# Performance work log

Measured on AMD Instinct MI355X. Metric: run time of the kernel, lower is better.

## Reference

```python
import jax, jax.numpy as jnp
import numpy as np

N_NODES = 100000
N_EDGES = 1600000
IN_DIM = 64
OUT_DIM = 64
BN_EPS = 1e-5


def batchnorm(h, gamma, beta):
    # BatchNorm1d in training mode: per-feature batch stats, biased variance
    mean = jnp.mean(h, axis=0)
    var = jnp.mean((h - mean) ** 2, axis=0)
    return gamma * (h - mean) * jax.lax.rsqrt(var + BN_EPS) + beta


def setup_inputs() -> dict:
    key = jax.random.key(0)
    ks = jax.random.split(key, 4)
    x = jax.random.normal(ks[0], (N_NODES, IN_DIM), dtype=jnp.float32)
    edge_index = jax.random.randint(ks[1], (2, N_EDGES), 0, N_NODES, dtype=jnp.int32)
    epsilon = jnp.asarray(0.1, dtype=jnp.float32)
    # Linear weights stored [in, out] (transpose of torch layout)
    W1 = jax.random.normal(ks[2], (IN_DIM, 2 * OUT_DIM), dtype=jnp.float32) * (1.0 / np.sqrt(IN_DIM))
    b1 = jnp.zeros((2 * OUT_DIM,), dtype=jnp.float32)
    g1 = jnp.ones((2 * OUT_DIM,), dtype=jnp.float32)
    be1 = jnp.zeros((2 * OUT_DIM,), dtype=jnp.float32)
    W2 = jax.random.normal(ks[3], (2 * OUT_DIM, OUT_DIM), dtype=jnp.float32) * (1.0 / np.sqrt(2 * OUT_DIM))
    b2 = jnp.zeros((OUT_DIM,), dtype=jnp.float32)
    g2 = jnp.ones((OUT_DIM,), dtype=jnp.float32)
    be2 = jnp.zeros((OUT_DIM,), dtype=jnp.float32)
    return {"x": x, "edge_index": edge_index, "epsilon": epsilon,
            "W1": W1, "b1": b1, "g1": g1, "be1": be1,
            "W2": W2, "b2": b2, "g2": g2, "be2": be2}


def reference(x, edge_index, epsilon, W1, b1, g1, be1, W2, b2, g2, be2):
    src, dst = edge_index[0], edge_index[1]
    # gather messages from src, scatter-add into dst  [N, D]
    neighbor_sum = jnp.zeros_like(x).at[dst].add(x[src])
    combined = (1.0 + epsilon) * x + neighbor_sum
    h = combined @ W1 + b1            # [N, 2*out_dim]
    h = jax.nn.relu(batchnorm(h, g1, be1))
    h = h @ W2 + b2                   # [N, out_dim]
    return batchnorm(h, g2, be2)
```

## Files before the change

kernel.cpp:

```cpp
#include <hip/hip_runtime.h>

#define N_NODES 100000
#define N_EDGES 1600000
#define IN_DIM 64
#define H_DIM 128
#define OUT_DIM 64
#define BN_EPS 1e-5f
#define CAP 64
#define BIN_SHIFT 9
#define BIN_NODES 512
#define NB 256
#define NBIN_BLOCKS ((N_NODES + BIN_NODES - 1) / BIN_NODES)

#define OFF_XB    0
#define OFF_COMB  3200000
#define OFF_H1    6400000
#define OFF_H2    12800000
#define OFF_STATS 19200000
#define S1SUM 0
#define S1SQ  128
#define S2SUM 256
#define S2SQ  320
#define STATS_FLOATS 768

#define DEV_ATOMIC_ADD(p, v) __hip_atomic_fetch_add((p), (v), __ATOMIC_RELAXED, __HIP_MEMORY_SCOPE_AGENT)

typedef __attribute__((ext_vector_type(8))) short short8;
typedef __attribute__((ext_vector_type(4))) float f32x4;

__device__ __forceinline__ unsigned short f2bf(float f) {
  union { float f; unsigned u; } v; v.f = f;
  unsigned r = v.u + 0x7FFFu + ((v.u >> 16) & 1u);
  return (unsigned short)(r >> 16);
}
__device__ __forceinline__ float bflo(unsigned v) { union { unsigned u; float f; } t; t.u = v << 16; return t.f; }
__device__ __forceinline__ float bfhi(unsigned v) { union { unsigned u; float f; } t; t.u = v & 0xFFFF0000u; return t.f; }

__global__ __launch_bounds__(256) void k_cvt(const float* __restrict__ x,
                                             unsigned short* __restrict__ xb) {
  int i = blockIdx.x * 256 + threadIdx.x;
  if (i < N_NODES * IN_DIM / 4) {
    float4 v = ((const float4*)x)[i];
    ushort4 o;
    o.x = f2bf(v.x); o.y = f2bf(v.y); o.z = f2bf(v.z); o.w = f2bf(v.w);
    *(ushort4*)(xb + i * 4) = o;
  }
}

__global__ __launch_bounds__(256) void k_bhist(const int* __restrict__ ei,
                                               int* __restrict__ bhist) {
  __shared__ int h[NB];
  const int tid = threadIdx.x;
  h[tid] = 0;
  __syncthreads();
  #pragma unroll
  for (int j = 0; j < 8; ++j) {
    int e = blockIdx.x * 2048 + j * 256 + tid;
    if (e < N_EDGES) atomicAdd(&h[ei[N_EDGES + e] >> BIN_SHIFT], 1);
  }
  __syncthreads();
  if (h[tid]) DEV_ATOMIC_ADD(&bhist[tid], h[tid]);
}

__global__ __launch_bounds__(256) void k_scan256(const int* __restrict__ bhist,
                                                 int* __restrict__ boff,
                                                 int* __restrict__ bcur) {
  __shared__ int s[NB];
  const int tid = threadIdx.x;
  int v = bhist[tid];
  s[tid] = v;
  __syncthreads();
  for (int d = 1; d < NB; d <<= 1) {
    int t = (tid >= d) ? s[tid - d] : 0;
    __syncthreads();
    s[tid] += t;
    __syncthreads();
  }
  int incl = s[tid];
  boff[tid] = incl - v;
  if (tid == NB - 1) boff[NB] = incl;
  bcur[tid] = incl - v;
}

__global__ __launch_bounds__(256) void k_bsplit(const int* __restrict__ ei,
                                                int* __restrict__ bcur,
                                                int2* __restrict__ binned) {
  __shared__ int lcnt[NB];
  __shared__ int lbase[NB];
  const int tid = threadIdx.x;
  lcnt[tid] = 0;
  __syncthreads();
  int src[8], dst[8], rk[8];
  #pragma unroll
  for (int j = 0; j < 8; ++j) {
    int e = blockIdx.x * 2048 + j * 256 + tid;
    if (e < N_EDGES) {
      src[j] = ei[e];
      dst[j] = ei[N_EDGES + e];
      rk[j] = atomicAdd(&lcnt[dst[j] >> BIN_SHIFT], 1);
    } else {
      src[j] = -1;
    }
  }
  __syncthreads();
  int c = lcnt[tid];
  if (c > 0) lbase[tid] = DEV_ATOMIC_ADD(&bcur[tid], c);
  __syncthreads();
  #pragma unroll
  for (int j = 0; j < 8; ++j) {
    if (src[j] >= 0) {
      int b = dst[j] >> BIN_SHIFT;
      binned[lbase[b] + rk[j]] = make_int2(src[j], dst[j]);
    }
  }
}

__global__ __launch_bounds__(512) void k_bfill(const int* __restrict__ boff,
                                               const int2* __restrict__ binned,
                                               int* __restrict__ cnt,
                                               int* __restrict__ srcl) {
  __shared__ int lcnt[BIN_NODES];
  const int tid = threadIdx.x;
  for (int i = tid; i < BIN_NODES; i += 512) lcnt[i] = 0;
  __syncthreads();
  const int b = blockIdx.x;
  const int s = boff[b], e = boff[b + 1];
  const int base = b * BIN_NODES;
  for (int i = s + tid; i < e; i += 512) {
    int2 ed = binned[i];
    int pos = atomicAdd(&lcnt[ed.y - base], 1);
    if (pos < CAP) srcl[ed.y * CAP + pos] = ed.x;
  }
  __syncthreads();
  for (int i = tid; i < BIN_NODES; i += 512) {
    int node = base + i;
    if (node < N_NODES) cnt[node] = lcnt[i];
  }
}

__global__ __launch_bounds__(256) void k_gather(const unsigned short* __restrict__ xb,
                                                const float* __restrict__ eps,
                                                const int* __restrict__ cnt,
                                                const int* __restrict__ srcl,
                                                unsigned short* __restrict__ comb) {
  int gid = blockIdx.x * 256 + threadIdx.x;
  int node = gid >> 3;
  int c = gid & 7;
  if (node >= N_NODES) return;
  float e = 1.0f + eps[0];
  uint4 u = *(const uint4*)(xb + node * 64 + c * 8);
  float a0 = bflo(u.x) * e, a1 = bfhi(u.x) * e;
  float a2 = bflo(u.y) * e, a3 = bfhi(u.y) * e;
  float a4 = bflo(u.z) * e, a5 = bfhi(u.z) * e;
  float a6 = bflo(u.w) * e, a7 = bfhi(u.w) * e;
  int deg = cnt[node];
  if (deg > CAP) deg = CAP;
  const int* sl = srcl + node * CAP;
  for (int j = 0; j < deg; ++j) {
    int s = sl[j];
    uint4 v = *(const uint4*)(xb + s * 64 + c * 8);
    a0 += bflo(v.x); a1 += bfhi(v.x);
    a2 += bflo(v.y); a3 += bfhi(v.y);
    a4 += bflo(v.z); a5 += bfhi(v.z);
    a6 += bflo(v.w); a7 += bfhi(v.w);
  }
  uint4 o;
  o.x = (unsigned)f2bf(a0) | ((unsigned)f2bf(a1) << 16);
  o.y = (unsigned)f2bf(a2) | ((unsigned)f2bf(a3) << 16);
  o.z = (unsigned)f2bf(a4) | ((unsigned)f2bf(a5) << 16);
  o.w = (unsigned)f2bf(a6) | ((unsigned)f2bf(a7) << 16);
  *(uint4*)(comb + node * 64 + c * 8) = o;
}

#define APAD 72
__global__ __launch_bounds__(256) void k_gemm1(const unsigned short* __restrict__ comb,
                                               const float* __restrict__ W1,
                                               const float* __restrict__ b1,
                                               unsigned short* __restrict__ h1,
                                               float* __restrict__ stats) {
  __shared__ unsigned short As[128 * APAD];
  __shared__ unsigned short Ws[128 * APAD];
  __shared__ float red[4][128];
  const int tid = threadIdx.x;
  const int wv = tid >> 6, lane = tid & 63;
  const int quad = lane >> 4, ln = lane & 15;
  const int rowBase = blockIdx.x * 128;

  #pragma unroll
  for (int it = 0; it < 4; ++it) {
    int idx = it * 256 + tid;
    int row = idx >> 3, ch = idx & 7;
    int gRow = rowBase + row;
    uint4 v = (gRow < N_NODES) ? *(const uint4*)(comb + gRow * 64 + ch * 8)
                               : make_uint4(0, 0, 0, 0);
    *(uint4*)&As[row * APAD + ch * 8] = v;
  }
  #pragma unroll
  for (int it = 0; it < 8; ++it) {
    int idx = it * 256 + tid;
    int k = idx >> 5, n4 = idx & 31;
    float4 wv1 = *(const float4*)(W1 + k * 128 + n4 * 4);
    Ws[(n4 * 4 + 0) * APAD + k] = f2bf(wv1.x);
    Ws[(n4 * 4 + 1) * APAD + k] = f2bf(wv1.y);
    Ws[(n4 * 4 + 2) * APAD + k] = f2bf(wv1.z);
    Ws[(n4 * 4 + 3) * APAD + k] = f2bf(wv1.w);
  }
  __syncthreads();

  f32x4 acc[2][8];
  #pragma unroll
  for (int mt = 0; mt < 2; ++mt) {
    #pragma unroll
    for (int nt = 0; nt < 8; ++nt) acc[mt][nt] = (f32x4)0.0f;
  }

  const int rw = wv * 32;
  #pragma unroll
  for (int kb = 0; kb < 2; ++kb) {
    short8 a0 = *(short8*)&As[(rw + ln) * APAD + kb * 32 + quad * 8];
    short8 a1 = *(short8*)&As[(rw + 16 + ln) * APAD + kb * 32 + quad * 8];
    #pragma unroll
    for (int nt = 0; nt < 8; ++nt) {
      short8 b = *(short8*)&Ws[(nt * 16 + ln) * APAD + kb * 32 + quad * 8];
      acc[0][nt] = __builtin_amdgcn_mfma_f32_16x16x32_bf16(a0, b, acc[0][nt], 0, 0, 0);
      acc[1][nt] = __builtin_amdgcn_mfma_f32_16x16x32_bf16(a1, b, acc[1][nt], 0, 0, 0);
    }
  }

  float bias[8], s[8], q[8];
  #pragma unroll
  for (int nt = 0; nt < 8; ++nt) { bias[nt] = b1[nt * 16 + ln]; s[nt] = 0.f; q[nt] = 0.f; }
  #pragma unroll
  for (int mt = 0; mt < 2; ++mt) {
    #pragma unroll
    for (int i = 0; i < 4; ++i) {
      int gRow = rowBase + rw + mt * 16 + quad * 4 + i;
      if (gRow < N_NODES) {
        #pragma unroll
        for (int nt = 0; nt < 8; ++nt) {
          float v = acc[mt][nt][i] + bias[nt];
          h1[gRow * 128 + nt * 16 + ln] = f2bf(v);
          s[nt] += v; q[nt] += v * v;
        }
      }
    }
  }
  #pragma unroll
  for (int nt = 0; nt < 8; ++nt) {
    s[nt] += __shfl_xor(s[nt], 16); s[nt] += __shfl_xor(s[nt], 32);
    q[nt] += __shfl_xor(q[nt], 16); q[nt] += __shfl_xor(q[nt], 32);
  }
  if (lane < 16) {
    #pragma unroll
    for (int nt = 0; nt < 8; ++nt) red[wv][nt * 16 + ln] = s[nt];
  }
  __syncthreads();
  if (tid < 128) DEV_ATOMIC_ADD(&stats[S1SUM + tid],
                                red[0][tid] + red[1][tid] + red[2][tid] + red[3][tid]);
  __syncthreads();
  if (lane < 16) {
    #pragma unroll
    for (int nt = 0; nt < 8; ++nt) red[wv][nt * 16 + ln] = q[nt];
  }
  __syncthreads();
  if (tid < 128) DEV_ATOMIC_ADD(&stats[S1SQ + tid],
                                red[0][tid] + red[1][tid] + red[2][tid] + red[3][tid]);
}

#define WPAD 136
__global__ __launch_bounds__(256) void k_gemm2(const unsigned short* __restrict__ h1,
                                               const float* __restrict__ W2,
                                               const float* __restrict__ b2,
                                               const float* __restrict__ g1,
                                               const float* __restrict__ be1,
                                               float* __restrict__ h2,
                                               float* __restrict__ stats) {
  __shared__ unsigned short As[128 * APAD];
  __shared__ unsigned short Ws[64 * WPAD];
  __shared__ float red[4][64];
  __shared__ float scL[128], shL[128];
  const int tid = threadIdx.x;
  const int wv = tid >> 6, lane = tid & 63;
  const int quad = lane >> 4, ln = lane & 15;
  const int rowBase = blockIdx.x * 128;

  if (tid < 128) {
    float mean = stats[S1SUM + tid] * (1.0f / N_NODES);
    float var = stats[S1SQ + tid] * (1.0f / N_NODES) - mean * mean;
    var = fmaxf(var, 0.0f);
    float sc = g1[tid] * rsqrtf(var + BN_EPS);
    scL[tid] = sc;
    shL[tid] = be1[tid] - mean * sc;
  }
  #pragma unroll
  for (int it = 0; it < 8; ++it) {
    int idx = it * 256 + tid;
    int k = idx >> 4, n4 = idx & 15;
    float4 wv2 = *(const float4*)(W2 + k * 64 + n4 * 4);
    Ws[(n4 * 4 + 0) * WPAD + k] = f2bf(wv2.x);
    Ws[(n4 * 4 + 1) * WPAD + k] = f2bf(wv2.y);
    Ws[(n4 * 4 + 2) * WPAD + k] = f2bf(wv2.z);
    Ws[(n4 * 4 + 3) * WPAD + k] = f2bf(wv2.w);
  }

  f32x4 acc[2][4];
  #pragma unroll
  for (int mt = 0; mt < 2; ++mt) {
    #pragma unroll
    for (int nt = 0; nt < 4; ++nt) acc[mt][nt] = (f32x4)0.0f;
  }
  const int rw = wv * 32;

  for (int kc = 0; kc < 2; ++kc) {
    __syncthreads();
    #pragma unroll
    for (int it = 0; it < 4; ++it) {
      int idx = it * 256 + tid;
      int row = idx >> 3, ch = idx & 7;
      int gRow = rowBase + row;
      uint4 u = (gRow < N_NODES) ? *(const uint4*)(h1 + gRow * 128 + kc * 64 + ch * 8)
                                 : make_uint4(0, 0, 0, 0);
      int kb = kc * 64 + ch * 8;
      float f0 = fmaxf(bflo(u.x) * scL[kb + 0] + shL[kb + 0], 0.f);
      float f1 = fmaxf(bfhi(u.x) * scL[kb + 1] + shL[kb + 1], 0.f);
      float f2 = fmaxf(bflo(u.y) * scL[kb + 2] + shL[kb + 2], 0.f);
      float f3 = fmaxf(bfhi(u.y) * scL[kb + 3] + shL[kb + 3], 0.f);
      float f4 = fmaxf(bflo(u.z) * scL[kb + 4] + shL[kb + 4], 0.f);
      float f5 = fmaxf(bfhi(u.z) * scL[kb + 5] + shL[kb + 5], 0.f);
      float f6 = fmaxf(bflo(u.w) * scL[kb + 6] + shL[kb + 6], 0.f);
      float f7 = fmaxf(bfhi(u.w) * scL[kb + 7] + shL[kb + 7], 0.f);
      uint4 o;
      o.x = (unsigned)f2bf(f0) | ((unsigned)f2bf(f1) << 16);
      o.y = (unsigned)f2bf(f2) | ((unsigned)f2bf(f3) << 16);
      o.z = (unsigned)f2bf(f4) | ((unsigned)f2bf(f5) << 16);
      o.w = (unsigned)f2bf(f6) | ((unsigned)f2bf(f7) << 16);
      *(uint4*)&As[row * APAD + ch * 8] = o;
    }
    __syncthreads();
    #pragma unroll
    for (int kb = 0; kb < 2; ++kb) {
      short8 a0 = *(short8*)&As[(rw + ln) * APAD + kb * 32 + quad * 8];
      short8 a1 = *(short8*)&As[(rw + 16 + ln) * APAD + kb * 32 + quad * 8];
      #pragma unroll
      for (int nt = 0; nt < 4; ++nt) {
        short8 b = *(short8*)&Ws[(nt * 16 + ln) * WPAD + kc * 64 + kb * 32 + quad * 8];
        acc[0][nt] = __builtin_amdgcn_mfma_f32_16x16x32_bf16(a0, b, acc[0][nt], 0, 0, 0);
        acc[1][nt] = __builtin_amdgcn_mfma_f32_16x16x32_bf16(a1, b, acc[1][nt], 0, 0, 0);
      }
    }
  }

  float bias[4], s[4], q[4];
  #pragma unroll
  for (int nt = 0; nt < 4; ++nt) { bias[nt] = b2[nt * 16 + ln]; s[nt] = 0.f; q[nt] = 0.f; }
  #pragma unroll
  for (int mt = 0; mt < 2; ++mt) {
    #pragma unroll
    for (int i = 0; i < 4; ++i) {
      int gRow = rowBase + rw + mt * 16 + quad * 4 + i;
      if (gRow < N_NODES) {
        #pragma unroll
        for (int nt = 0; nt < 4; ++nt) {
          float v = acc[mt][nt][i] + bias[nt];
          h2[gRow * 64 + nt * 16 + ln] = v;
          s[nt] += v; q[nt] += v * v;
        }
      }
    }
  }
  #pragma unroll
  for (int nt = 0; nt < 4; ++nt) {
    s[nt] += __shfl_xor(s[nt], 16); s[nt] += __shfl_xor(s[nt], 32);
    q[nt] += __shfl_xor(q[nt], 16); q[nt] += __shfl_xor(q[nt], 32);
  }
  if (lane < 16) {
    #pragma unroll
    for (int nt = 0; nt < 4; ++nt) red[wv][nt * 16 + ln] = s[nt];
  }
  __syncthreads();
  if (tid < 64) DEV_ATOMIC_ADD(&stats[S2SUM + tid],
                               red[0][tid] + red[1][tid] + red[2][tid] + red[3][tid]);
  __syncthreads();
  if (lane < 16) {
    #pragma unroll
    for (int nt = 0; nt < 4; ++nt) red[wv][nt * 16 + ln] = q[nt];
  }
  __syncthreads();
  if (tid < 64) DEV_ATOMIC_ADD(&stats[S2SQ + tid],
                               red[0][tid] + red[1][tid] + red[2][tid] + red[3][tid]);
}

__global__ __launch_bounds__(256) void k_out(const float* __restrict__ h2,
                                             const float* __restrict__ stats,
                                             const float* __restrict__ g2,
                                             const float* __restrict__ be2,
                                             float* __restrict__ out) {
  __shared__ float scL[64], shL[64];
  const int tid = threadIdx.x;
  if (tid < 64) {
    float mean = stats[S2SUM + tid] * (1.0f / N_NODES);
    float var = stats[S2SQ + tid] * (1.0f / N_NODES) - mean * mean;
    var = fmaxf(var, 0.0f);
    float sc = g2[tid] * rsqrtf(var + BN_EPS);
    scL[tid] = sc;
    shL[tid] = be2[tid] - mean * sc;
  }
  __syncthreads();
  int i = blockIdx.x * 256 + tid;
  if (i < N_NODES * OUT_DIM / 4) {
    int c = i & 15;
    float4 v = ((const float4*)h2)[i];
    float4 sc = ((const float4*)scL)[c];
    float4 sh = ((const float4*)shL)[c];
    v.x = v.x * sc.x + sh.x;
    v.y = v.y * sc.y + sh.y;
    v.z = v.z * sc.z + sh.z;
    v.w = v.w * sc.w + sh.w;
    ((float4*)out)[i] = v;
  }
}

extern "C" void kernel_launch(void* const* d_in, const int* in_sizes, int n_in,
                              void* d_out, int out_size, void* d_ws, size_t ws_size,
                              hipStream_t stream) {
  const float* x   = (const float*)d_in[0];
  const int*   ei  = (const int*)d_in[1];
  const float* eps = (const float*)d_in[2];
  const float* W1  = (const float*)d_in[3];
  const float* b1  = (const float*)d_in[4];
  const float* g1  = (const float*)d_in[5];
  const float* be1 = (const float*)d_in[6];
  const float* W2  = (const float*)d_in[7];
  const float* b2  = (const float*)d_in[8];
  const float* g2  = (const float*)d_in[9];
  const float* be2 = (const float*)d_in[10];

  float* ws = (float*)d_ws;
  unsigned short* xb   = (unsigned short*)(ws + OFF_XB);
  unsigned short* comb = (unsigned short*)(ws + OFF_COMB);
  int2*           binned = (int2*)(ws + OFF_COMB);
  unsigned short* h1   = (unsigned short*)(ws + OFF_H1);
  int*            srcl = (int*)(ws + OFF_H1);
  float*          h2   = ws + OFF_H2;
  int*            cnt  = (int*)(ws + OFF_H2);
  int*            bhist = cnt + N_NODES;
  int*            boff  = bhist + NB;
  int*            bcur  = boff + NB + 7;
  float*          stats = ws + OFF_STATS;
  float*          out   = (float*)d_out;

  hipMemsetAsync(stats, 0, STATS_FLOATS * sizeof(float), stream);
  hipMemsetAsync(bhist, 0, NB * sizeof(int), stream);

  const int edgeGrid = (N_EDGES + 2047) / 2048;
  const int gemmGrid = (N_NODES + 127) / 128;
  k_cvt<<<(N_NODES * IN_DIM / 4 + 255) / 256, 256, 0, stream>>>(x, xb);
  k_bhist<<<edgeGrid, 256, 0, stream>>>(ei, bhist);
  k_scan256<<<1, NB, 0, stream>>>(bhist, boff, bcur);
  k_bsplit<<<edgeGrid, 256, 0, stream>>>(ei, bcur, binned);
  k_bfill<<<NBIN_BLOCKS, 512, 0, stream>>>(boff, binned, cnt, srcl);
  k_gather<<<(N_NODES * 8 + 255) / 256, 256, 0, stream>>>(xb, eps, cnt, srcl, comb);
  k_gemm1<<<gemmGrid, 256, 0, stream>>>(comb, W1, b1, h1, stats);
  k_gemm2<<<gemmGrid, 256, 0, stream>>>(h1, W2, b2, g1, be1, h2, stats);
  k_out<<<(N_NODES * OUT_DIM / 4 + 255) / 256, 256, 0, stream>>>(h2, stats, g2, be2, out);
}
```

Before: 282.0 us.

## Stage binned edges in LDS, widen gather lanes, store h2 in bf16

k_bsplit now writes its edges into shared memory sorted by bin via a local prefix scan, then copies them out, so global writes of binned edges are grouped by bin and more contiguous. k_gather uses 4 threads per node with 32-byte loads and handles two neighbours per loop iteration, which cuts thread count and raises the number of loads in flight per thread. The second GEMM writes h2 as bf16 instead of fp32, and k_out reads bf16, halving the traffic of that intermediate. The costs are lower precision in the pre-BN2 output, extra shared-memory scan work in bsplit, and more registers in gather.

```diff
diff --git a/kernel.cpp b/kernel.cpp
--- a/kernel.cpp
+++ b/kernel.cpp
@@ -36,6 +36,19 @@
 __device__ __forceinline__ float bflo(unsigned v) { union { unsigned u; float f; } t; t.u = v << 16; return t.f; }
 __device__ __forceinline__ float bfhi(unsigned v) { union { unsigned u; float f; } t; t.u = v & 0xFFFF0000u; return t.f; }
 
+__device__ __forceinline__ void acc8(float* a, uint4 v) {
+  a[0] += bflo(v.x); a[1] += bfhi(v.x); a[2] += bflo(v.y); a[3] += bfhi(v.y);
+  a[4] += bflo(v.z); a[5] += bfhi(v.z); a[6] += bflo(v.w); a[7] += bfhi(v.w);
+}
+__device__ __forceinline__ uint4 pack8(const float* a) {
+  uint4 o;
+  o.x = (unsigned)f2bf(a[0]) | ((unsigned)f2bf(a[1]) << 16);
+  o.y = (unsigned)f2bf(a[2]) | ((unsigned)f2bf(a[3]) << 16);
+  o.z = (unsigned)f2bf(a[4]) | ((unsigned)f2bf(a[5]) << 16);
+  o.w = (unsigned)f2bf(a[6]) | ((unsigned)f2bf(a[7]) << 16);
+  return o;
+}
+
 __global__ __launch_bounds__(256) void k_cvt(const float* __restrict__ x,
                                              unsigned short* __restrict__ xb) {
   int i = blockIdx.x * 256 + threadIdx.x;
@@ -86,7 +99,10 @@
                                                 int* __restrict__ bcur,
                                                 int2* __restrict__ binned) {
   __shared__ int lcnt[NB];
+  __shared__ int lofs[NB];
   __shared__ int lbase[NB];
+  __shared__ int sc[NB];
+  __shared__ int2 staged[2048];
   const int tid = threadIdx.x;
   lcnt[tid] = 0;
   __syncthreads();
@@ -103,15 +119,31 @@
     }
   }
   __syncthreads();
-  int c = lcnt[tid];
-  if (c > 0) lbase[tid] = DEV_ATOMIC_ADD(&bcur[tid], c);
+  int v = lcnt[tid];
+  sc[tid] = v;
+  __syncthreads();
+  for (int d = 1; d < NB; d <<= 1) {
+    int t = (tid >= d) ? sc[tid - d] : 0;
+    __syncthreads();
+    sc[tid] += t;
+    __syncthreads();
+  }
+  lofs[tid] = sc[tid] - v;
+  if (v > 0) lbase[tid] = DEV_ATOMIC_ADD(&bcur[tid], v);
   __syncthreads();
   #pragma unroll
   for (int j = 0; j < 8; ++j) {
     if (src[j] >= 0) {
       int b = dst[j] >> BIN_SHIFT;
-      binned[lbase[b] + rk[j]] = make_int2(src[j], dst[j]);
-    }
+      staged[lofs[b] + rk[j]] = make_int2(src[j], dst[j]);
+    }
+  }
+  int nv = sc[NB - 1];
+  __syncthreads();
+  for (int i = tid; i < nv; i += 256) {
+    int2 e = staged[i];
+    int b = e.y >> BIN_SHIFT;
+    binned[lbase[b] + (i - lofs[b])] = e;
   }
 }
 
@@ -144,32 +176,41 @@
                                                 const int* __restrict__ srcl,
                                                 unsigned short* __restrict__ comb) {
   int gid = blockIdx.x * 256 + threadIdx.x;
-  int node = gid >> 3;
-  int c = gid & 7;
+  int node = gid >> 2;
+  int c = gid & 3;
   if (node >= N_NODES) return;
+  float a[16];
+  #pragma unroll
+  for (int i = 0; i < 16; ++i) a[i] = 0.f;
+  const unsigned short* bp = xb + node * 64 + c * 16;
+  acc8(a, *(const uint4*)bp);
+  acc8(a + 8, *(const uint4*)(bp + 8));
   float e = 1.0f + eps[0];
-  uint4 u = *(const uint4*)(xb + node * 64 + c * 8);
-  float a0 = bflo(u.x) * e, a1 = bfhi(u.x) * e;
-  float a2 = bflo(u.y) * e, a3 = bfhi(u.y) * e;
-  float a4 = bflo(u.z) * e, a5 = bfhi(u.z) * e;
-  float a6 = bflo(u.w) * e, a7 = bfhi(u.w) * e;
+  #pragma unroll
+  for (int i = 0; i < 16; ++i) a[i] *= e;
   int deg = cnt[node];
   if (deg > CAP) deg = CAP;
   const int* sl = srcl + node * CAP;
-  for (int j = 0; j < deg; ++j) {
-    int s = sl[j];
-    uint4 v = *(const uint4*)(xb + s * 64 + c * 8);
-    a0 += bflo(v.x); a1 += bfhi(v.x);
-    a2 += bflo(v.y); a3 += bfhi(v.y);
-    a4 += bflo(v.z); a5 += bfhi(v.z);
-    a6 += bflo(v.w); a7 += bfhi(v.w);
-  }
-  uint4 o;
-  o.x = (unsigned)f2bf(a0) | ((unsigned)f2bf(a1) << 16);
-  o.y = (unsigned)f2bf(a2) | ((unsigned)f2bf(a3) << 16);
-  o.z = (unsigned)f2bf(a4) | ((unsigned)f2bf(a5) << 16);
-  o.w = (unsigned)f2bf(a6) | ((unsigned)f2bf(a7) << 16);
-  *(uint4*)(comb + node * 64 + c * 8) = o;
+  int j = 0;
+  for (; j + 2 <= deg; j += 2) {
+    int s0 = sl[j], s1 = sl[j + 1];
+    const unsigned short* p0 = xb + s0 * 64 + c * 16;
+    const unsigned short* p1 = xb + s1 * 64 + c * 16;
+    uint4 v0 = *(const uint4*)p0;
+    uint4 v1 = *(const uint4*)(p0 + 8);
+    uint4 w0 = *(const uint4*)p1;
+    uint4 w1 = *(const uint4*)(p1 + 8);
+    acc8(a, v0); acc8(a + 8, v1);
+    acc8(a, w0); acc8(a + 8, w1);
+  }
+  if (j < deg) {
+    const unsigned short* p0 = xb + sl[j] * 64 + c * 16;
+    acc8(a, *(const uint4*)p0);
+    acc8(a + 8, *(const uint4*)(p0 + 8));
+  }
+  unsigned short* op = comb + node * 64 + c * 16;
+  *(uint4*)op = pack8(a);
+  *(uint4*)(op + 8) = pack8(a + 8);
 }
 
 #define APAD 72
@@ -213,7 +254,6 @@
     #pragma unroll
     for (int nt = 0; nt < 8; ++nt) acc[mt][nt] = (f32x4)0.0f;
   }
-
   const int rw = wv * 32;
   #pragma unroll
   for (int kb = 0; kb < 2; ++kb) {
@@ -273,7 +313,7 @@
                                                const float* __restrict__ b2,
                                                const float* __restrict__ g1,
                                                const float* __restrict__ be1,
-                                               float* __restrict__ h2,
+                                               unsigned short* __restrict__ h2,
                                                float* __restrict__ stats) {
   __shared__ unsigned short As[128 * APAD];
   __shared__ unsigned short Ws[64 * WPAD];
@@ -362,7 +402,7 @@
         #pragma unroll
         for (int nt = 0; nt < 4; ++nt) {
           float v = acc[mt][nt][i] + bias[nt];
-          h2[gRow * 64 + nt * 16 + ln] = v;
+          h2[gRow * 64 + nt * 16 + ln] = f2bf(v);
           s[nt] += v; q[nt] += v * v;
         }
       }
@@ -390,7 +430,7 @@
                                red[0][tid] + red[1][tid] + red[2][tid] + red[3][tid]);
 }
 
-__global__ __launch_bounds__(256) void k_out(const float* __restrict__ h2,
+__global__ __launch_bounds__(256) void k_out(const unsigned short* __restrict__ h2,
                                              const float* __restrict__ stats,
                                              const float* __restrict__ g2,
                                              const float* __restrict__ be2,
@@ -409,7 +449,8 @@
   int i = blockIdx.x * 256 + tid;
   if (i < N_NODES * OUT_DIM / 4) {
     int c = i & 15;
-    float4 v = ((const float4*)h2)[i];
+    uint2 u = *(const uint2*)(h2 + i * 4);
+    float4 v = {bflo(u.x), bfhi(u.x), bflo(u.y), bfhi(u.y)};
     float4 sc = ((const float4*)scL)[c];
     float4 sh = ((const float4*)shL)[c];
     v.x = v.x * sc.x + sh.x;
@@ -441,7 +482,7 @@
   int2*           binned = (int2*)(ws + OFF_COMB);
   unsigned short* h1   = (unsigned short*)(ws + OFF_H1);
   int*            srcl = (int*)(ws + OFF_H1);
-  float*          h2   = ws + OFF_H2;
+  unsigned short* h2   = (unsigned short*)(ws + OFF_H2);
   int*            cnt  = (int*)(ws + OFF_H2);
   int*            bhist = cnt + N_NODES;
   int*            boff  = bhist + NB;
@@ -459,7 +500,7 @@
   k_scan256<<<1, NB, 0, stream>>>(bhist, boff, bcur);
   k_bsplit<<<edgeGrid, 256, 0, stream>>>(ei, bcur, binned);
   k_bfill<<<NBIN_BLOCKS, 512, 0, stream>>>(boff, binned, cnt, srcl);
-  k_gather<<<(N_NODES * 8 + 255) / 256, 256, 0, stream>>>(xb, eps, cnt, srcl, comb);
+  k_gather<<<(N_NODES * 4 + 255) / 256, 256, 0, stream>>>(xb, eps, cnt, srcl, comb);
   k_gemm1<<<gemmGrid, 256, 0, stream>>>(comb, W1, b1, h1, stats);
   k_gemm2<<<gemmGrid, 256, 0, stream>>>(h1, W2, b2, g1, be1, h2, stats);
   k_out<<<(N_NODES * OUT_DIM / 4 + 255) / 256, 256, 0, stream>>>(h2, stats, g2, be2, out);
```

Measured after the change: 272.4 us. -3.4%, faster.
